# Kernel optimization log

Hardware: AMD Instinct MI355X
Metric: run time of the kernel (lower is better)

Reference implementation:

```python
import jax, jax.numpy as jnp
import numpy as np
from jax import lax

B, N, C_IN, C_OUT = 8, 8192, 64, 128
NUM_SAMPLES, K = 2048, 32
EPS = 1e-5


def _bn(x, g, b, m, v):
    # inference-mode BatchNorm1d over channel axis 1; x: [G, C, L]
    scale = g / jnp.sqrt(v + EPS)
    return (x - m[None, :, None]) * scale[None, :, None] + b[None, :, None]


def _conv1x1(x, w):
    # kernel_size=1 Conv1d (no bias); x: [G, Cin, L], w: [Cout, Cin]
    return jnp.einsum('gck,oc->gok', x, w)


def _res_block(x, w1, g1, b1, m1, v1, w2, g2, b2, m2, v2):
    # conv-bn-relu -> conv-bn, residual add, relu (residual_factor=1.0)
    y = jax.nn.relu(_bn(_conv1x1(x, w1), g1, b1, m1, v1))
    y = _bn(_conv1x1(y, w2), g2, b2, m2, v2)
    return jax.nn.relu(y + x)


def _fps(xyz, num_samples):
    # farthest point sampling; xyz: [B,N,3] -> indices [B,S]
    b, n, _ = xyz.shape

    def step(carry, _):
        dists, last_idx = carry
        last_pt = jnp.take_along_axis(xyz, last_idx[:, None, None], axis=1)  # [B,1,3]
        d = jnp.sum((xyz - last_pt) ** 2, axis=-1)  # [B,N]
        dists = jnp.minimum(dists, d)
        nxt = jnp.argmax(dists, axis=-1).astype(jnp.int32)
        return (dists, nxt), last_idx

    init = (jnp.full((b, n), 1e10, xyz.dtype), jnp.zeros((b,), jnp.int32))
    _, idxs = lax.scan(step, init, None, length=num_samples)
    return jnp.transpose(idxs)  # [B,S]


def setup_inputs():
    key = jax.random.key(0)
    ks = jax.random.split(key, 40)
    xyz = jax.random.uniform(ks[0], (B, N, 3), jnp.float32)
    feat = jax.random.normal(ks[1], (B, N, C_IN), jnp.float32)

    def conv_w(k, o, c):
        return jax.random.normal(k, (o, c), jnp.float32) * (1.0 / np.sqrt(c).astype(np.float32))

    def bn_params(k, c):
        k1, k2, k3, k4 = jax.random.split(k, 4)
        return (1.0 + 0.1 * jax.random.normal(k1, (c,), jnp.float32),
                0.1 * jax.random.normal(k2, (c,), jnp.float32),
                0.1 * jax.random.normal(k3, (c,), jnp.float32),
                jax.random.uniform(k4, (c,), jnp.float32, 0.5, 1.5))

    inp = {'xyz': xyz, 'feat': feat}
    inp['te_w'] = conv_w(ks[2], C_OUT, 2 * C_IN)
    inp['te_g'], inp['te_b'], inp['te_m'], inp['te_v'] = bn_params(ks[3], C_OUT)
    for name, base in (('pre', 4), ('pos', 14)):
        inp[name + '_w1'] = jnp.stack([conv_w(ks[base + i], C_OUT, C_OUT) for i in range(2)])
        inp[name + '_w2'] = jnp.stack([conv_w(ks[base + 2 + i], C_OUT, C_OUT) for i in range(2)])
        bn1 = [bn_params(ks[base + 4 + i], C_OUT) for i in range(2)]
        bn2 = [bn_params(ks[base + 6 + i], C_OUT) for i in range(2)]
        for j, s in enumerate(('g', 'b', 'm', 'v')):
            inp[f'{name}_{s}1'] = jnp.stack([bn1[i][j] for i in range(2)])
            inp[f'{name}_{s}2'] = jnp.stack([bn2[i][j] for i in range(2)])
    return inp


def reference(xyz, feat, te_w, te_g, te_b, te_m, te_v,
              pre_w1, pre_w2, pre_g1, pre_b1, pre_m1, pre_v1, pre_g2, pre_b2, pre_m2, pre_v2,
              pos_w1, pos_w2, pos_g1, pos_b1, pos_m1, pos_v1, pos_g2, pos_b2, pos_m2, pos_v2):
    bsz = xyz.shape[0]
    # --- LocalGrouper: FPS centers + kNN grouping + concat center feat ---
    fps_idx = _fps(xyz, NUM_SAMPLES)                                    # [B,S]
    new_xyz = jnp.take_along_axis(xyz, fps_idx[..., None], axis=1)      # [B,S,3]
    ctr_feat = jnp.take_along_axis(feat, fps_idx[..., None], axis=1)    # [B,S,C]
    d2 = jnp.sum((new_xyz[:, :, None, :] - xyz[:, None, :, :]) ** 2, axis=-1)  # [B,S,N]
    _, knn_idx = lax.top_k(-d2, K)                                      # [B,S,K]
    grouped = feat[jnp.arange(bsz)[:, None, None], knn_idx]             # [B,S,K,C]
    ctr = jnp.broadcast_to(ctr_feat[:, :, None, :], grouped.shape)
    nf = jnp.concatenate([grouped, ctr], axis=-1)                       # [B,S,K,2C]
    # --- permute/view -> [B*S, 2C, K] ---
    x = nf.transpose(0, 1, 3, 2).reshape(bsz * NUM_SAMPLES, 2 * C_IN, K)
    x = jax.nn.relu(_bn(_conv1x1(x, te_w), te_g, te_b, te_m, te_v))     # [G,OUT,K]
    for i in range(2):
        x = _res_block(x, pre_w1[i], pre_g1[i], pre_b1[i], pre_m1[i], pre_v1[i],
                       pre_w2[i], pre_g2[i], pre_b2[i], pre_m2[i], pre_v2[i])
    x = jnp.max(x, axis=-1)                                             # adaptive_max_pool1d(.,1)
    x = x.reshape(bsz, NUM_SAMPLES, C_OUT).transpose(0, 2, 1)           # [B,OUT,S]
    for i in range(2):
        x = _res_block(x, pos_w1[i], pos_g1[i], pos_b1[i], pos_m1[i], pos_v1[i],
                       pos_w2[i], pos_g2[i], pos_b2[i], pos_m2[i], pos_v2[i])
    return new_xyz, x
```

## Files before the change

kernel.cpp:

```cpp
#include <hip/hip_runtime.h>

typedef unsigned short u16;
typedef unsigned int   u32;
typedef unsigned long long u64;

#define B_    8
#define N_    8192
#define CIN   64
#define COUT  128
#define NS    2048
#define K_    32
#define LDSPAD 136

typedef __attribute__((ext_vector_type(8))) short short8;
typedef __attribute__((ext_vector_type(4))) float f32x4;
typedef __attribute__((ext_vector_type(2))) float f32x2;

#define MFMA16(a,b,c) __builtin_amdgcn_mfma_f32_16x16x32_bf16(a,b,c,0,0,0)

__device__ __forceinline__ u16 f2bf(float f){
  u32 u = __float_as_uint(f);
  return (u16)((u + 0x7FFFu + ((u >> 16) & 1u)) >> 16);
}
__device__ __forceinline__ float bf2f(u16 h){ u32 u = ((u32)h) << 16; return __uint_as_float(u); }
__device__ __forceinline__ u32 pack2bf(float lo, float hi){ return (u32)f2bf(lo) | ((u32)f2bf(hi) << 16); }

__global__ void wcvt_kernel(const float* __restrict__ s, u16* __restrict__ d, int n){
  int i = blockIdx.x * 256 + threadIdx.x;
  if (i < n) d[i] = f2bf(s[i]);
}

__global__ void clear_kernel(int* __restrict__ fps_idx, u32* __restrict__ done){
  int i = blockIdx.x * 256 + threadIdx.x;
  if (i < B_*NS){ fps_idx[i] = -1; done[i] = 0u; }
}

struct BnPtrs { const float* g[9]; const float* b[9]; const float* m[9]; const float* v[9]; };

__global__ void bn_pre_kernel(BnPtrs p, float* __restrict__ bns){
  int set = blockIdx.x, c = threadIdx.x;
  float sc = p.g[set][c] / sqrtf(p.v[set][c] + 1e-5f);
  bns[set*256 + c]       = sc;
  bns[set*256 + 128 + c] = p.b[set][c] - p.m[set][c] * sc;
}

struct ShFps {
  __align__(16) f32x4 PX4[4*512];
  __align__(16) f32x4 PY4[4*512];
  __align__(16) f32x4 PZ4[4*512];
  u64  keyA[2][8];
  __align__(16) f32x4 cA[2][8];
};
struct ShMid {
  __align__(16) u16 X[8][32*LDSPAD];
  __align__(16) float scr[8][128];
};
struct ShPos {
  __align__(16) u16 X[8][32*LDSPAD];
};
union ShAll { ShFps f; ShMid m; ShPos p; };

#define DPP_UMAX(x, ctrl) { \
  u32 o = (u32)__builtin_amdgcn_update_dpp((int)(x), (int)(x), ctrl, 0xf, 0xf, false); \
  x = (o > x) ? o : x; }

__device__ __forceinline__ u32 wave_umax63(u32 x){
  DPP_UMAX(x, 0x111)
  DPP_UMAX(x, 0x112)
  DPP_UMAX(x, 0x114)
  DPP_UMAX(x, 0x118)
  DPP_UMAX(x, 0x142)
  DPP_UMAX(x, 0x143)
  return (u32)__builtin_amdgcn_readlane((int)x, 63);
}

#define FPS_PAIR(m) { \
  f32x2 dx = PXr##m - lx2; \
  f32x2 dy = PYr##m - ly2; \
  f32x2 dz = PZr##m - lz2; \
  f32x2 t0 = dx*dx; \
  f32x2 t1 = dy*dy; \
  f32x2 t2 = dz*dz; \
  f32x2 dd = (t0 + t1) + t2; \
  f32x2 nd; \
  nd.x = fminf(Dr##m.x, dd.x); \
  nd.y = fminf(Dr##m.y, dd.y); \
  Dr##m = nd; \
  fmA = fmaxf(fmA, nd.x); \
  fmB = fmaxf(fmB, nd.y); }

#define FPS_KMIN2(m) { \
  if (Dr##m.y == wmf) kk = 2*m + 1; \
  if (Dr##m.x == wmf) kk = 2*m; }

__device__ __forceinline__ void selmax(u64& ka, f32x4& ca, u64 kb, f32x4 cb){
  bool c = kb > ka;
  ka = c ? kb : ka;
  ca = c ? cb : ca;
}

__device__ void fps_path(const float* __restrict__ xyz, int* __restrict__ fps_idx,
                         ShFps& S, int b, int t){
  #pragma clang fp contract(off)
  const int lane = t & 63, wv = t >> 6;
  const float* xb = xyz + (size_t)b * N_ * 3;
  f32x4* PX4 = S.PX4; f32x4* PY4 = S.PY4; f32x4* PZ4 = S.PZ4;
  const int base = t * 16;
  #pragma unroll
  for (int j = 0; j < 4; ++j){
    f32x4 xv, yv, zv;
    #pragma unroll
    for (int i = 0; i < 4; ++i){
      const int p = base + 4*j + i;
      xv[i] = xb[p*3 + 0];
      yv[i] = xb[p*3 + 1];
      zv[i] = xb[p*3 + 2];
    }
    PX4[j*512 + t] = xv; PY4[j*512 + t] = yv; PZ4[j*512 + t] = zv;
  }
  if (t == 0)
    __hip_atomic_store(fps_idx + b*NS, 0, __ATOMIC_RELAXED, __HIP_MEMORY_SCOPE_AGENT);
  __syncthreads();
  const float* PXs = (const float*)PX4;
  const float* PYs = (const float*)PY4;
  const float* PZs = (const float*)PZ4;
  f32x2 PXr0,PXr1,PXr2,PXr3,PXr4,PXr5,PXr6,PXr7;
  f32x2 PYr0,PYr1,PYr2,PYr3,PYr4,PYr5,PYr6,PYr7;
  f32x2 PZr0,PZr1,PZr2,PZr3,PZr4,PZr5,PZr6,PZr7;
  #define LOADP(jj, a, bq) { \
    f32x4 vx = PX4[jj*512 + t]; f32x4 vy = PY4[jj*512 + t]; f32x4 vz = PZ4[jj*512 + t]; \
    PXr##a.x = vx[0]; PXr##a.y = vx[1]; PXr##bq.x = vx[2]; PXr##bq.y = vx[3]; \
    PYr##a.x = vy[0]; PYr##a.y = vy[1]; PYr##bq.x = vy[2]; PYr##bq.y = vy[3]; \
    PZr##a.x = vz[0]; PZr##a.y = vz[1]; PZr##bq.x = vz[2]; PZr##bq.y = vz[3]; }
  LOADP(0,0,1) LOADP(1,2,3) LOADP(2,4,5) LOADP(3,6,7)
  #undef LOADP
  f32x2 Dr0,Dr1,Dr2,Dr3,Dr4,Dr5,Dr6,Dr7;
  Dr0=Dr1=Dr2=Dr3=Dr4=Dr5=Dr6=Dr7=(f32x2){1e10f,1e10f};
  float sx = PXs[0], sy = PYs[0], sz = PZs[0];
  f32x2 lx2 = {sx,sx}, ly2 = {sy,sy}, lz2 = {sz,sz};
  int my_pi = 0;
  for (int s = 0; s < NS - 1; ++s){
    float fmA = 0.f, fmB = 0.f;
    FPS_PAIR(0) FPS_PAIR(1) FPS_PAIR(2) FPS_PAIR(3)
    FPS_PAIR(4) FPS_PAIR(5) FPS_PAIR(6) FPS_PAIR(7)
    const float fm = fmaxf(fmA, fmB);
    const u32 tbm = __float_as_uint(fm);
    const u32 wmax = wave_umax63(tbm);
    const u64 mask = __ballot(tbm == wmax);
    const int fl = __ffsll((long long)mask) - 1;
    const int sl = s & 1;
    if (lane == fl){
      const float wmf = __uint_as_float(wmax);
      int kk = 0;
      FPS_KMIN2(7) FPS_KMIN2(6) FPS_KMIN2(5) FPS_KMIN2(4)
      FPS_KMIN2(3) FPS_KMIN2(2) FPS_KMIN2(1) FPS_KMIN2(0)
      const int pi = base + kk;
      const int li = (kk >> 2)*2048 + t*4 + (kk & 3);
      S.keyA[sl][wv] = ((u64)wmax << 13) | (u64)(8191 - pi);
      f32x4 c; c[0] = PXs[li]; c[1] = PYs[li]; c[2] = PZs[li]; c[3] = 0.f;
      S.cA[sl][wv] = c;
    }
    __syncthreads();
    u64 k0 = S.keyA[sl][0], k1 = S.keyA[sl][1], k2 = S.keyA[sl][2], k3 = S.keyA[sl][3];
    u64 k4 = S.keyA[sl][4], k5 = S.keyA[sl][5], k6 = S.keyA[sl][6], k7 = S.keyA[sl][7];
    f32x4 c0 = S.cA[sl][0], c1 = S.cA[sl][1], c2 = S.cA[sl][2], c3 = S.cA[sl][3];
    f32x4 c4 = S.cA[sl][4], c5 = S.cA[sl][5], c6 = S.cA[sl][6], c7 = S.cA[sl][7];
    selmax(k0,c0,k1,c1); selmax(k2,c2,k3,c3); selmax(k4,c4,k5,c5); selmax(k6,c6,k7,c7);
    selmax(k0,c0,k2,c2); selmax(k4,c4,k6,c6);
    selmax(k0,c0,k4,c4);
    lx2.x = c0[0]; lx2.y = c0[0];
    ly2.x = c0[1]; ly2.y = c0[1];
    lz2.x = c0[2]; lz2.y = c0[2];
    const int pi_out = 8191 - (int)(k0 & 0x1FFFull);
    if (lane == (s & 15)) my_pi = pi_out;
    if ((s & 15) == 15 && t < 16)
      __hip_atomic_store(fps_idx + b*NS + s - 14 + t, my_pi,
                         __ATOMIC_RELAXED, __HIP_MEMORY_SCOPE_AGENT);
  }
  if (t < 15)
    __hip_atomic_store(fps_idx + b*NS + (NS - 15) + t, my_pi,
                       __ATOMIC_RELAXED, __HIP_MEMORY_SCOPE_AGENT);
}

__device__ __forceinline__ void zero_acc(f32x4 acc[8][2]){
  #pragma unroll
  for (int mt = 0; mt < 8; ++mt)
    #pragma unroll
    for (int nt = 0; nt < 2; ++nt){
      acc[mt][nt][0] = 0.f; acc[mt][nt][1] = 0.f; acc[mt][nt][2] = 0.f; acc[mt][nt][3] = 0.f;
    }
}

__device__ __forceinline__ void conv_step(const u16* __restrict__ W, const u16* __restrict__ Xw,
                                          int q, int l15, f32x4 acc[8][2]){
  #pragma unroll
  for (int kk = 0; kk < 4; ++kk){
    short8 b0 = *(const short8*)(Xw + l15*LDSPAD + kk*32 + q*8);
    short8 b1 = *(const short8*)(Xw + (16 + l15)*LDSPAD + kk*32 + q*8);
    #pragma unroll
    for (int mt = 0; mt < 8; ++mt){
      short8 a = *(const short8*)(W + (size_t)(mt*16 + l15)*COUT + kk*32 + q*8);
      acc[mt][0] = MFMA16(a, b0, acc[mt][0]);
      acc[mt][1] = MFMA16(a, b1, acc[mt][1]);
    }
  }
}

__device__ __forceinline__ void res_block(const u16* __restrict__ W1, const u16* __restrict__ W2,
    const float* __restrict__ bn1, const float* __restrict__ bn2,
    u16* __restrict__ Xw, int q, int l15, u32 resid[8][2][2], f32x4 acc[8][2], bool writeback){
  zero_acc(acc);
  conv_step(W1, Xw, q, l15, acc);
  #pragma unroll
  for (int mt = 0; mt < 8; ++mt){
    f32x4 sc = *(const f32x4*)(bn1 + mt*16 + q*4);
    f32x4 bi = *(const f32x4*)(bn1 + 128 + mt*16 + q*4);
    #pragma unroll
    for (int nt = 0; nt < 2; ++nt){
      float y0 = fmaxf(fmaf(acc[mt][nt][0], sc[0], bi[0]), 0.f);
      float y1 = fmaxf(fmaf(acc[mt][nt][1], sc[1], bi[1]), 0.f);
      float y2 = fmaxf(fmaf(acc[mt][nt][2], sc[2], bi[2]), 0.f);
      float y3 = fmaxf(fmaf(acc[mt][nt][3], sc[3], bi[3]), 0.f);
      *(uint2*)(Xw + (nt*16 + l15)*LDSPAD + mt*16 + q*4) = make_uint2(pack2bf(y0,y1), pack2bf(y2,y3));
    }
  }
  __syncthreads();
  zero_acc(acc);
  conv_step(W2, Xw, q, l15, acc);
  #pragma unroll
  for (int mt = 0; mt < 8; ++mt){
    f32x4 sc = *(const f32x4*)(bn2 + mt*16 + q*4);
    f32x4 bi = *(const f32x4*)(bn2 + 128 + mt*16 + q*4);
    #pragma unroll
    for (int nt = 0; nt < 2; ++nt){
      float r0 = bf2f((u16)(resid[mt][nt][0] & 0xFFFFu));
      float r1 = bf2f((u16)(resid[mt][nt][0] >> 16));
      float r2 = bf2f((u16)(resid[mt][nt][1] & 0xFFFFu));
      float r3 = bf2f((u16)(resid[mt][nt][1] >> 16));
      float y0 = fmaxf(fmaf(acc[mt][nt][0], sc[0], bi[0]) + r0, 0.f);
      float y1 = fmaxf(fmaf(acc[mt][nt][1], sc[1], bi[1]) + r1, 0.f);
      float y2 = fmaxf(fmaf(acc[mt][nt][2], sc[2], bi[2]) + r2, 0.f);
      float y3 = fmaxf(fmaf(acc[mt][nt][3], sc[3], bi[3]) + r3, 0.f);
      acc[mt][nt][0] = y0; acc[mt][nt][1] = y1; acc[mt][nt][2] = y2; acc[mt][nt][3] = y3;
      if (writeback){
        u32 p0 = pack2bf(y0,y1), p1 = pack2bf(y2,y3);
        resid[mt][nt][0] = p0; resid[mt][nt][1] = p1;
        *(uint2*)(Xw + (nt*16 + l15)*LDSPAD + mt*16 + q*4) = make_uint2(p0, p1);
      }
    }
  }
  if (writeback) __syncthreads();
}

__device__ void knnmid_path(const float* __restrict__ xyz, const float* __restrict__ feat,
    const u16* __restrict__ te_w, const u16* __restrict__ pre_w1, const u16* __restrict__ pre_w2,
    const float* __restrict__ bns, int* __restrict__ fps_idx,
    u16* __restrict__ x_mid, u32* __restrict__ done, float* __restrict__ out_xyz,
    u16* __restrict__ Xw, float* __restrict__ scrw, int g, int lane){
  #pragma clang fp contract(off)
  const int b = g >> 11;
  const float* xb = xyz + (size_t)b * N_ * 3;

  int raw;
  for (;;){
    raw = __hip_atomic_load(fps_idx + g, __ATOMIC_RELAXED, __HIP_MEMORY_SCOPE_AGENT);
    if (raw >= 0) break;
    __builtin_amdgcn_s_sleep(2);
  }
  const int ci = raw & (N_ - 1);
  const float cx = xb[ci*3], cy = xb[ci*3+1], cz = xb[ci*3+2];
  if (lane < 3) out_xyz[g*3 + lane] = xb[ci*3 + lane];

  float rd = __uint_as_float(0x7F800000u); int ri = 0x7FFFFFFF;
  float r31d = rd; int r31i = ri;
  for (int c = 0; c < N_/64; ++c){
    const int pid = c*64 + lane;
    float dx = xb[pid*3]   - cx;
    float dy = xb[pid*3+1] - cy;
    float dz = xb[pid*3+2] - cz;
    float t0 = dx*dx, t1 = dy*dy, t2 = dz*dz;
    float d2 = (t0 + t1) + t2;
    u64 m = __ballot((d2 < r31d) || (d2 == r31d && pid < r31i));
    while (m){
      int l = __ffsll((long long)m) - 1; m &= m - 1;
      float v = __shfl(d2, l); int vi = c*64 + l;
      if (!((v < r31d) || (v == r31d && vi < r31i))) continue;
      bool lt = (rd < v) || (rd == v && ri < vi);
      int pos = __popcll(__ballot(lt));
      float prd = __shfl_up(rd, 1); int pri = __shfl_up(ri, 1);
      if (lane == pos){ rd = v; ri = vi; }
      else if (lane > pos){ rd = prd; ri = pri; }
      r31d = __shfl(rd, 31); r31i = __shfl(ri, 31);
    }
  }

  const int q = lane >> 4, l15 = lane & 15;
  const float* fb = feat + (size_t)b * N_ * CIN;
  #pragma unroll
  for (int it = 0; it < 4; ++it){
    int lidx = it*64 + lane;
    int kq = lidx & 7;
    int col = it*8 + (lane >> 3);
    int nb = __shfl(ri, col) & (N_ - 1);
    f32x4 a0 = *(const f32x4*)(fb + (size_t)nb*CIN + kq*8);
    f32x4 a1 = *(const f32x4*)(fb + (size_t)nb*CIN + kq*8 + 4);
    *(uint2*)(Xw + col*LDSPAD + kq*8)     = make_uint2(pack2bf(a0[0],a0[1]), pack2bf(a0[2],a0[3]));
    *(uint2*)(Xw + col*LDSPAD + kq*8 + 4) = make_uint2(pack2bf(a1[0],a1[1]), pack2bf(a1[2],a1[3]));
    f32x4 c0 = *(const f32x4*)(fb + (size_t)ci*CIN + kq*8);
    f32x4 c1 = *(const f32x4*)(fb + (size_t)ci*CIN + kq*8 + 4);
    *(uint2*)(Xw + col*LDSPAD + 64 + kq*8)     = make_uint2(pack2bf(c0[0],c0[1]), pack2bf(c0[2],c0[3]));
    *(uint2*)(Xw + col*LDSPAD + 64 + kq*8 + 4) = make_uint2(pack2bf(c1[0],c1[1]), pack2bf(c1[2],c1[3]));
  }
  __syncthreads();

  f32x4 acc[8][2];
  u32 resid[8][2][2];
  zero_acc(acc);
  conv_step(te_w, Xw, q, l15, acc);
  #pragma unroll
  for (int mt = 0; mt < 8; ++mt){
    f32x4 sc = *(const f32x4*)(bns + mt*16 + q*4);
    f32x4 bi = *(const f32x4*)(bns + 128 + mt*16 + q*4);
    #pragma unroll
    for (int nt = 0; nt < 2; ++nt){
      float y0 = fmaxf(fmaf(acc[mt][nt][0], sc[0], bi[0]), 0.f);
      float y1 = fmaxf(fmaf(acc[mt][nt][1], sc[1], bi[1]), 0.f);
      float y2 = fmaxf(fmaf(acc[mt][nt][2], sc[2], bi[2]), 0.f);
      float y3 = fmaxf(fmaf(acc[mt][nt][3], sc[3], bi[3]), 0.f);
      u32 p0 = pack2bf(y0,y1), p1 = pack2bf(y2,y3);
      resid[mt][nt][0] = p0; resid[mt][nt][1] = p1;
      *(uint2*)(Xw + (nt*16 + l15)*LDSPAD + mt*16 + q*4) = make_uint2(p0, p1);
    }
  }
  __syncthreads();

  res_block(pre_w1,             pre_w2,             bns + 256, bns + 512,  Xw, q, l15, resid, acc, true);
  res_block(pre_w1 + COUT*COUT, pre_w2 + COUT*COUT, bns + 768, bns + 1024, Xw, q, l15, resid, acc, false);

  float mx[8][4];
  #pragma unroll
  for (int mt = 0; mt < 8; ++mt)
    #pragma unroll
    for (int r = 0; r < 4; ++r){
      float m0 = fmaxf(acc[mt][0][r], acc[mt][1][r]);
      #pragma unroll
      for (int off = 1; off < 16; off <<= 1) m0 = fmaxf(m0, __shfl_xor(m0, off));
      mx[mt][r] = m0;
    }
  if (l15 == 0){
    #pragma unroll
    for (int mt = 0; mt < 8; ++mt){
      f32x4 vv; vv[0] = mx[mt][0]; vv[1] = mx[mt][1]; vv[2] = mx[mt][2]; vv[3] = mx[mt][3];
      *(f32x4*)(scrw + mt*16 + q*4) = vv;
    }
  }
  __syncthreads();
  float v0 = scrw[lane*2], v1 = scrw[lane*2 + 1];
  *(u32*)(x_mid + (size_t)g*COUT + lane*2) = pack2bf(v0, v1);
  if (lane == 0)
    __hip_atomic_store(done + g, 1u, __ATOMIC_RELEASE, __HIP_MEMORY_SCOPE_AGENT);
}

__device__ void pos_path(const u16* __restrict__ x_mid,
    const u16* __restrict__ pos_w1, const u16* __restrict__ pos_w2,
    const float* __restrict__ bns, float* __restrict__ out_x,
    u32* __restrict__ done, u16* __restrict__ Xw, int g, int lane){
  const int q = lane >> 4, l15 = lane & 15;
  const int gc0 = g * 32;
  const int b = gc0 >> 11, s0 = gc0 & 2047;
  for (;;){
    u32 d = (lane < 32)
      ? __hip_atomic_load(done + gc0 + lane, __ATOMIC_RELAXED, __HIP_MEMORY_SCOPE_AGENT)
      : 1u;
    if (__all(d != 0)) break;
    __builtin_amdgcn_s_sleep(16);
  }
  __builtin_amdgcn_fence(__ATOMIC_ACQUIRE, "agent");
  #pragma unroll
  for (int it = 0; it < 8; ++it){
    int lidx = it*64 + lane;
    int col = lidx >> 4, kq = lidx & 15;
    uint4 v = *(const uint4*)(x_mid + (size_t)(gc0 + col)*COUT + kq*8);
    *(uint4*)(Xw + col*LDSPAD + kq*8) = v;
  }
  __syncthreads();
  u32 resid[8][2][2];
  #pragma unroll
  for (int mt = 0; mt < 8; ++mt)
    #pragma unroll
    for (int nt = 0; nt < 2; ++nt){
      uint2 rr = *(const uint2*)(Xw + (nt*16 + l15)*LDSPAD + mt*16 + q*4);
      resid[mt][nt][0] = rr.x; resid[mt][nt][1] = rr.y;
    }
  f32x4 acc[8][2];
  res_block(pos_w1,             pos_w2,             bns + 1280, bns + 1536, Xw, q, l15, resid, acc, true);
  res_block(pos_w1 + COUT*COUT, pos_w2 + COUT*COUT, bns + 1792, bns + 2048, Xw, q, l15, resid, acc, false);
  #pragma unroll
  for (int mt = 0; mt < 8; ++mt)
    #pragma unroll
    for (int nt = 0; nt < 2; ++nt)
      #pragma unroll
      for (int r = 0; r < 4; ++r){
        int row = mt*16 + q*4 + r;
        int colx = s0 + nt*16 + l15;
        out_x[(size_t)(b*COUT + row)*NS + colx] = acc[mt][nt][r];
      }
}

#define GRID_FPS    B_
#define GRID_KM     (B_*NS/8)
#define GRID_POS    (B_*NS/K_/8)

__global__ __launch_bounds__(512) void mega_kernel(
    const float* __restrict__ xyz, const float* __restrict__ feat,
    const u16* __restrict__ te_w, const u16* __restrict__ pre_w1, const u16* __restrict__ pre_w2,
    const u16* __restrict__ pos_w1, const u16* __restrict__ pos_w2,
    const float* __restrict__ bns, int* __restrict__ fps_idx,
    u16* __restrict__ x_mid, u32* __restrict__ done,
    float* __restrict__ out_xyz, float* __restrict__ out_x){
  __shared__ ShAll sh;
  const int bid = blockIdx.x;
  const int t = threadIdx.x;
  const int wid = t >> 6, lane = t & 63;
  if (bid < GRID_FPS){
    fps_path(xyz, fps_idx, sh.f, bid, t);
  } else if (bid < GRID_FPS + GRID_KM){
    const int g0 = (bid - GRID_FPS)*8;
    if (t == 0){
      while (__hip_atomic_load(fps_idx + g0 + 7, __ATOMIC_RELAXED,
                               __HIP_MEMORY_SCOPE_AGENT) < 0)
        __builtin_amdgcn_s_sleep(16);
    }
    __syncthreads();
    knnmid_path(xyz, feat, te_w, pre_w1, pre_w2, bns, fps_idx, x_mid, done, out_xyz,
                sh.m.X[wid], sh.m.scr[wid], g0 + wid, lane);
  } else {
    const int g = (bid - GRID_FPS - GRID_KM)*8 + wid;
    pos_path(x_mid, pos_w1, pos_w2, bns, out_x, done, sh.p.X[wid], g, lane);
  }
}

extern "C" void kernel_launch(void* const* d_in, const int* in_sizes, int n_in,
                              void* d_out, int out_size, void* d_ws, size_t ws_size,
                              hipStream_t stream){
  (void)in_sizes; (void)n_in; (void)out_size; (void)ws_size;
  const float* xyz    = (const float*)d_in[0];
  const float* feat   = (const float*)d_in[1];

  char* ws = (char*)d_ws;
  float* bns     = (float*)ws;
  u16*   wbf     = (u16*)(ws + 16384);
  int*   fps_idx = (int*)(ws + 16384 + 294912);
  u32*   done    = (u32*)(ws + 16384 + 294912 + 65536);
  u16*   x_mid   = (u16*)(ws + 16384 + 294912 + 65536 + 65536);
  float* out_xyz = (float*)d_out;
  float* out_x   = (float*)d_out + B_*NS*3;

  u16* te_w   = wbf;
  u16* pre_w1 = wbf + 16384;
  u16* pre_w2 = wbf + 49152;
  u16* pos_w1 = wbf + 81920;
  u16* pos_w2 = wbf + 114688;
  wcvt_kernel<<<64,  256, 0, stream>>>((const float*)d_in[2],  te_w,   16384);
  wcvt_kernel<<<128, 256, 0, stream>>>((const float*)d_in[7],  pre_w1, 32768);
  wcvt_kernel<<<128, 256, 0, stream>>>((const float*)d_in[8],  pre_w2, 32768);
  wcvt_kernel<<<128, 256, 0, stream>>>((const float*)d_in[17], pos_w1, 32768);
  wcvt_kernel<<<128, 256, 0, stream>>>((const float*)d_in[18], pos_w2, 32768);
  clear_kernel<<<64, 256, 0, stream>>>(fps_idx, done);

  BnPtrs bp;
  const int gi[9] = {3, 9, 10, 9, 10, 19, 20, 19, 20};
  const int bbi[9]= {4, 11,12, 11,12, 21, 22, 21, 22};
  const int mi[9] = {5, 13,14, 13,14, 23, 24, 23, 24};
  const int vi[9] = {6, 15,16, 15,16, 25, 26, 25, 26};
  const int of[9] = {0, 0, 0, 128,128, 0, 0, 128,128};
  for (int k = 0; k < 9; ++k){
    bp.g[k] = (const float*)d_in[gi[k]]  + of[k];
    bp.b[k] = (const float*)d_in[bbi[k]] + of[k];
    bp.m[k] = (const float*)d_in[mi[k]]  + of[k];
    bp.v[k] = (const float*)d_in[vi[k]]  + of[k];
  }

  bn_pre_kernel<<<9, 128, 0, stream>>>(bp, bns);
  mega_kernel<<<GRID_FPS + GRID_KM + GRID_POS, 512, 0, stream>>>(
      xyz, feat, te_w, pre_w1, pre_w2, pos_w1, pos_w2, bns,
      fps_idx, x_mid, done, out_xyz, out_x);
}
```

Baseline: 3.029 ms.

## Keep FPS points in registers, lighten barrier, interleave consumer blocks across batches

FPS blocks now load their 16 points per thread straight from global memory into registers with vector loads, dropping the LDS staging arrays. The winning coordinates are taken from registers instead of an LDS lookup, and the per-step __syncthreads is replaced with a bare lgkmcnt wait plus s_barrier. The LDS union is padded to a fixed size. KNN and pos blocks are re-mapped so that consecutive blocks cycle across batches, letting consumers start on all eight FPS streams in parallel instead of waiting on batch 0 first. This risks a different load/occupancy balance and relies on the hand-written barrier being a sufficient fence.

New measurement: 2.812 ms (median of 2 runs). 1.08x faster.

```diff
diff --git a/kernel.cpp b/kernel.cpp
--- a/kernel.cpp
+++ b/kernel.cpp
@@ -45,10 +45,7 @@
 }
 
 struct ShFps {
-  __align__(16) f32x4 PX4[4*512];
-  __align__(16) f32x4 PY4[4*512];
-  __align__(16) f32x4 PZ4[4*512];
-  u64  keyA[2][8];
+  __align__(16) u64  keyA[2][8];
   __align__(16) f32x4 cA[2][8];
 };
 struct ShMid {
@@ -58,7 +55,13 @@
 struct ShPos {
   __align__(16) u16 X[8][32*LDSPAD];
 };
-union ShAll { ShFps f; ShMid m; ShPos p; };
+union ShAll { ShFps f; ShMid m; ShPos p; char pad[83968]; };
+
+__device__ __forceinline__ void lds_barrier(){
+  __builtin_amdgcn_sched_barrier(0);
+  asm volatile("s_waitcnt lgkmcnt(0)\n\ts_barrier" ::: "memory");
+  __builtin_amdgcn_sched_barrier(0);
+}
 
 #define DPP_UMAX(x, ctrl) { \
   u32 o = (u32)__builtin_amdgcn_update_dpp((int)(x), (int)(x), ctrl, 0xf, 0xf, false); \
@@ -89,9 +92,9 @@
   fmA = fmaxf(fmA, nd.x); \
   fmB = fmaxf(fmB, nd.y); }
 
-#define FPS_KMIN2(m) { \
-  if (Dr##m.y == wmf) kk = 2*m + 1; \
-  if (Dr##m.x == wmf) kk = 2*m; }
+#define FPS_SELK(m) { \
+  if (Dr##m.y == wmf){ kk = 2*m + 1; wx = PXr##m.y; wy = PYr##m.y; wz = PZr##m.y; } \
+  if (Dr##m.x == wmf){ kk = 2*m;     wx = PXr##m.x; wy = PYr##m.x; wz = PZr##m.x; } }
 
 __device__ __forceinline__ void selmax(u64& ka, f32x4& ca, u64 kb, f32x4 cb){
   bool c = kb > ka;
@@ -104,39 +107,32 @@
   #pragma clang fp contract(off)
   const int lane = t & 63, wv = t >> 6;
   const float* xb = xyz + (size_t)b * N_ * 3;
-  f32x4* PX4 = S.PX4; f32x4* PY4 = S.PY4; f32x4* PZ4 = S.PZ4;
   const int base = t * 16;
-  #pragma unroll
-  for (int j = 0; j < 4; ++j){
-    f32x4 xv, yv, zv;
-    #pragma unroll
-    for (int i = 0; i < 4; ++i){
-      const int p = base + 4*j + i;
-      xv[i] = xb[p*3 + 0];
-      yv[i] = xb[p*3 + 1];
-      zv[i] = xb[p*3 + 2];
-    }
-    PX4[j*512 + t] = xv; PY4[j*512 + t] = yv; PZ4[j*512 + t] = zv;
-  }
-  if (t == 0)
-    __hip_atomic_store(fps_idx + b*NS, 0, __ATOMIC_RELAXED, __HIP_MEMORY_SCOPE_AGENT);
-  __syncthreads();
-  const float* PXs = (const float*)PX4;
-  const float* PYs = (const float*)PY4;
-  const float* PZs = (const float*)PZ4;
+  f32x4 raw0, raw1, raw2, raw3, raw4, raw5, raw6, raw7, raw8, raw9, rawA, rawB;
+  {
+    const f32x4* xv = (const f32x4*)(xb + (size_t)base * 3);
+    raw0 = xv[0]; raw1 = xv[1]; raw2 = xv[2];  raw3 = xv[3];
+    raw4 = xv[4]; raw5 = xv[5]; raw6 = xv[6];  raw7 = xv[7];
+    raw8 = xv[8]; raw9 = xv[9]; rawA = xv[10]; rawB = xv[11];
+  }
   f32x2 PXr0,PXr1,PXr2,PXr3,PXr4,PXr5,PXr6,PXr7;
   f32x2 PYr0,PYr1,PYr2,PYr3,PYr4,PYr5,PYr6,PYr7;
   f32x2 PZr0,PZr1,PZr2,PZr3,PZr4,PZr5,PZr6,PZr7;
-  #define LOADP(jj, a, bq) { \
-    f32x4 vx = PX4[jj*512 + t]; f32x4 vy = PY4[jj*512 + t]; f32x4 vz = PZ4[jj*512 + t]; \
-    PXr##a.x = vx[0]; PXr##a.y = vx[1]; PXr##bq.x = vx[2]; PXr##bq.y = vx[3]; \
-    PYr##a.x = vy[0]; PYr##a.y = vy[1]; PYr##bq.x = vy[2]; PYr##bq.y = vy[3]; \
-    PZr##a.x = vz[0]; PZr##a.y = vz[1]; PZr##bq.x = vz[2]; PZr##bq.y = vz[3]; }
-  LOADP(0,0,1) LOADP(1,2,3) LOADP(2,4,5) LOADP(3,6,7)
-  #undef LOADP
+  #define GETF(k) (k<4?raw0[(k)&3]:k<8?raw1[(k)&3]:k<12?raw2[(k)&3]:k<16?raw3[(k)&3]: \
+                   k<20?raw4[(k)&3]:k<24?raw5[(k)&3]:k<28?raw6[(k)&3]:k<32?raw7[(k)&3]: \
+                   k<36?raw8[(k)&3]:k<40?raw9[(k)&3]:k<44?rawA[(k)&3]:rawB[(k)&3])
+  #define SETP(m) { \
+    PXr##m.x = GETF(6*m+0); PXr##m.y = GETF(6*m+3); \
+    PYr##m.x = GETF(6*m+1); PYr##m.y = GETF(6*m+4); \
+    PZr##m.x = GETF(6*m+2); PZr##m.y = GETF(6*m+5); }
+  SETP(0) SETP(1) SETP(2) SETP(3) SETP(4) SETP(5) SETP(6) SETP(7)
+  #undef SETP
+  #undef GETF
+  if (t == 0)
+    __hip_atomic_store(fps_idx + b*NS, 0, __ATOMIC_RELAXED, __HIP_MEMORY_SCOPE_AGENT);
   f32x2 Dr0,Dr1,Dr2,Dr3,Dr4,Dr5,Dr6,Dr7;
   Dr0=Dr1=Dr2=Dr3=Dr4=Dr5=Dr6=Dr7=(f32x2){1e10f,1e10f};
-  float sx = PXs[0], sy = PYs[0], sz = PZs[0];
+  const float sx = xb[0], sy = xb[1], sz = xb[2];
   f32x2 lx2 = {sx,sx}, ly2 = {sy,sy}, lz2 = {sz,sz};
   int my_pi = 0;
   for (int s = 0; s < NS - 1; ++s){
@@ -152,15 +148,15 @@
     if (lane == fl){
       const float wmf = __uint_as_float(wmax);
       int kk = 0;
-      FPS_KMIN2(7) FPS_KMIN2(6) FPS_KMIN2(5) FPS_KMIN2(4)
-      FPS_KMIN2(3) FPS_KMIN2(2) FPS_KMIN2(1) FPS_KMIN2(0)
+      float wx = PXr0.x, wy = PYr0.x, wz = PZr0.x;
+      FPS_SELK(7) FPS_SELK(6) FPS_SELK(5) FPS_SELK(4)
+      FPS_SELK(3) FPS_SELK(2) FPS_SELK(1) FPS_SELK(0)
       const int pi = base + kk;
-      const int li = (kk >> 2)*2048 + t*4 + (kk & 3);
       S.keyA[sl][wv] = ((u64)wmax << 13) | (u64)(8191 - pi);
-      f32x4 c; c[0] = PXs[li]; c[1] = PYs[li]; c[2] = PZs[li]; c[3] = 0.f;
+      f32x4 c; c[0] = wx; c[1] = wy; c[2] = wz; c[3] = 0.f;
       S.cA[sl][wv] = c;
     }
-    __syncthreads();
+    lds_barrier();
     u64 k0 = S.keyA[sl][0], k1 = S.keyA[sl][1], k2 = S.keyA[sl][2], k3 = S.keyA[sl][3];
     u64 k4 = S.keyA[sl][4], k5 = S.keyA[sl][5], k6 = S.keyA[sl][6], k7 = S.keyA[sl][7];
     f32x4 c0 = S.cA[sl][0], c1 = S.cA[sl][1], c2 = S.cA[sl][2], c3 = S.cA[sl][3];
@@ -425,7 +421,8 @@
   if (bid < GRID_FPS){
     fps_path(xyz, fps_idx, sh.f, bid, t);
   } else if (bid < GRID_FPS + GRID_KM){
-    const int g0 = (bid - GRID_FPS)*8;
+    const int i = bid - GRID_FPS;
+    const int g0 = (i & 7) * NS + (i >> 3) * 8;
     if (t == 0){
       while (__hip_atomic_load(fps_idx + g0 + 7, __ATOMIC_RELAXED,
                                __HIP_MEMORY_SCOPE_AGENT) < 0)
@@ -435,7 +432,8 @@
     knnmid_path(xyz, feat, te_w, pre_w1, pre_w2, bns, fps_idx, x_mid, done, out_xyz,
                 sh.m.X[wid], sh.m.scr[wid], g0 + wid, lane);
   } else {
-    const int g = (bid - GRID_FPS - GRID_KM)*8 + wid;
+    const int idx = (bid - GRID_FPS - GRID_KM)*8 + wid;
+    const int g = (idx & 7) * (NS/K_) + (idx >> 3);
     pos_path(x_mid, pos_w1, pos_w2, bns, out_x, done, sh.p.X[wid], g, lane);
   }
 }
```
